# Kernel optimization log

Measured on AMD Instinct MI355X. Metric: run time of the kernel, lower is better.

The kernel has to match this reference:

```python
import jax, jax.numpy as jnp
import numpy as np
from jax import lax

B, S, H, D, NH, L, NC = 64, 512, 64, 128, 8, 4, 5
DT = 0.01

def _xavier(key, shape, gain=0.1):
    a = gain * np.sqrt(6.0 / (shape[0] + shape[1]))
    return jax.random.uniform(key, shape, jnp.float32, -a, a)

def setup_inputs():
    key = jax.random.key(0)
    ks = jax.random.split(key, 20)
    # strictly increasing positive times with spacing exactly dt -> one Euler step per interval
    times = (jnp.arange(S, dtype=jnp.float32) + 1.0) * DT
    feats = jax.random.uniform(ks[0], (B, S, 2), jnp.float32, 0.5, 5.0)
    time_series = jnp.concatenate([jnp.broadcast_to(times[None, :, None], (B, S, 1)), feats], axis=2)
    mask = jnp.ones((B, S), dtype=bool)
    noise = jax.random.normal(ks[1], (S - 1, B, H), jnp.float32)  # standard normal; scaled by sqrt(dt) inside
    n = lambda k, sh: 0.02 * jax.random.normal(k, sh, jnp.float32)
    return dict(
        time_series=time_series, mask=mask, noise=noise,
        dW1=_xavier(ks[2], (H + 1, 2 * H)), db1=jnp.zeros(2 * H, jnp.float32),
        dW2=_xavier(ks[3], (2 * H, H)), db2=jnp.zeros(H, jnp.float32),
        dW3=_xavier(ks[4], (H, H)), db3=jnp.zeros(H, jnp.float32),
        gW1=_xavier(ks[5], (H + 1, 2 * H)), gb1=jnp.zeros(2 * H, jnp.float32),
        gW2=_xavier(ks[6], (2 * H, H)), gb2=jnp.zeros(H, jnp.float32),
        min_diffusion=jnp.float32(0.05), max_drift=jnp.float32(1.0),
        in_W=n(ks[7], (H, D)), in_b=jnp.zeros(D, jnp.float32),
        Wq=n(ks[8], (L, D, D)), bq=jnp.zeros((L, D), jnp.float32),
        Wk=n(ks[9], (L, D, D)), bk=jnp.zeros((L, D), jnp.float32),
        Wv=n(ks[10], (L, D, D)), bv=jnp.zeros((L, D), jnp.float32),
        Wo=n(ks[11], (L, D, D)), bo=jnp.zeros((L, D), jnp.float32),
        ln1_s=jnp.ones((L, D), jnp.float32), ln1_b=jnp.zeros((L, D), jnp.float32),
        fW1=n(ks[12], (L, D, 4 * D)), fb1=jnp.zeros((L, 4 * D), jnp.float32),
        fW2=n(ks[13], (L, 4 * D, D)), fb2=jnp.zeros((L, D), jnp.float32),
        ln2_s=jnp.ones((L, D), jnp.float32), ln2_b=jnp.zeros((L, D), jnp.float32),
        cW1=n(ks[14], (D, D // 2)), cb1=jnp.zeros(D // 2, jnp.float32),
        cW2=n(ks[15], (D // 2, NC)), cb2=jnp.zeros(NC, jnp.float32),
    )

def _ln(x, s, b):
    m = x.mean(-1, keepdims=True)
    v = ((x - m) ** 2).mean(-1, keepdims=True)
    return (x - m) * lax.rsqrt(v + 1e-5) * s + b

def reference(time_series, mask, noise, dW1, db1, dW2, db2, dW3, db3,
              gW1, gb1, gW2, gb2, min_diffusion, max_drift,
              in_W, in_b, Wq, bq, Wk, bk, Wv, bv, Wo, bo,
              ln1_s, ln1_b, fW1, fb1, fW2, fb2, ln2_s, ln2_b,
              cW1, cb1, cW2, cb2):
    b, s = time_series.shape[:2]
    h = dW3.shape[1]
    nin = min(3, h)  # min(input_dim, hidden_channels)
    times = time_series[:, :, 0]

    # initial SDE state
    y0 = jnp.full((b, h), 0.1, time_series.dtype)
    y0 = y0.at[:, :nin].set(jnp.clip(time_series[:, 0, :nin], 0.01, 10.0))

    # per-interval left times, step sizes, Brownian increments (batch-shared time, element 0)
    ts0 = times[0]                        # (S,)
    t_left = ts0[:-1]                     # (S-1,)
    hstep = ts0[1:] - ts0[:-1]            # (S-1,)
    dW = noise * jnp.sqrt(hstep)[:, None, None]  # (S-1, B, H)

    def euler_step(y, inp):
        t, hh, dw = inp
        t_col = jnp.broadcast_to(jnp.reshape(t, (1, 1)), (y.shape[0], 1))
        ty = jnp.concatenate([y, t_col], axis=1)              # (B, H+1)
        # drift coeff net: Linear-Tanh-Linear-Tanh-Linear, clamped
        dc = jnp.tanh(ty @ dW1 + db1)
        dc = jnp.tanh(dc @ dW2 + db2)
        dc = dc @ dW3 + db3
        dc = jnp.clip(dc, -jnp.abs(max_drift), jnp.abs(max_drift))
        f = dc * y
        # diffusion coeff net: Linear-Tanh-Linear-Softplus + |min_diffusion|
        gc = jnp.tanh(ty @ gW1 + gb1)
        gc = jax.nn.softplus(gc @ gW2 + gb2) + jnp.abs(min_diffusion)
        g = gc * jnp.clip(y, -10.0, 10.0)
        y1 = jnp.clip(y + f * hh + g * dw, 0.01, 10.0)  # Euler-Maruyama + post-solve clamp
        return y1, y1

    _, traj = lax.scan(euler_step, y0, (t_left, hstep, dW))   # (S-1, B, H)
    sde_features = jnp.concatenate([y0[None], traj], axis=0).transpose(1, 0, 2)  # (B, S, H)
    mf = mask[..., None].astype(sde_features.dtype)
    sde_features = sde_features * mf

    # ContiFormer (standard post-LN transformer encoder over SDE features)
    x = sde_features @ in_W + in_b                            # (B, S, D)
    d = x.shape[-1]
    dh = d // NH
    scale = 1.0 / np.sqrt(dh)
    neg = jnp.asarray(-1e9, x.dtype)
    for l in range(Wq.shape[0]):
        q = (x @ Wq[l] + bq[l]).reshape(b, s, NH, dh)
        k = (x @ Wk[l] + bk[l]).reshape(b, s, NH, dh)
        v = (x @ Wv[l] + bv[l]).reshape(b, s, NH, dh)
        scores = jnp.einsum('bqhd,bkhd->bhqk', q, k) * scale
        scores = jnp.where(mask[:, None, None, :], scores, neg)
        attn = jax.nn.softmax(scores, axis=-1)
        o = jnp.einsum('bhqk,bkhd->bqhd', attn, v).reshape(b, s, d) @ Wo[l] + bo[l]
        x = _ln(x + o, ln1_s[l], ln1_b[l])
        ff = jax.nn.relu(x @ fW1[l] + fb1[l]) @ fW2[l] + fb2[l]
        x = _ln(x + ff, ln2_s[l], ln2_b[l])

    pooled = (x * mf).sum(1) / jnp.maximum(mf.sum(1), 1.0)    # masked mean pool (B, D)
    logits = jax.nn.relu(pooled @ cW1 + cb1) @ cW2 + cb2      # (B, NC)
    return (logits, sde_features)
```

## Files before the change

### kernel.cpp

```cpp
#include <hip/hip_runtime.h>
#include <hip/hip_bf16.h>
#include <math.h>

#define BB 64
#define SS 512
#define HH 64
#define DD 128
#define NHD 8
#define ROWS (BB*SS)

typedef unsigned short u16;
typedef __attribute__((ext_vector_type(8))) short bf16x8;
typedef __attribute__((ext_vector_type(4))) float f32x4;

__device__ __forceinline__ u16 f2b(float f) {
  union { float f; unsigned u; } x; x.f = f;
  unsigned r = x.u + 0x7fffu + ((x.u >> 16) & 1u);
  return (u16)(r >> 16);
}

__device__ __forceinline__ float b2f(u16 u) {
  return __uint_as_float(((unsigned)u) << 16);
}

__device__ __forceinline__ float fast_tanh(float x) {
  float ax = fminf(fabsf(x), 15.f);
  float e = __expf(2.f * ax);
  float r = 1.f - __fdividef(2.f, e + 1.f);
  return copysignf(r, x);
}

__device__ __forceinline__ void barrier_lds() {
  __builtin_amdgcn_s_waitcnt(0xC07F);
  __builtin_amdgcn_s_barrier();
}

__global__ __launch_bounds__(512, 2) void sde_kernel(
    const float* __restrict__ ts, const float* __restrict__ noise,
    const float* __restrict__ dW1, const float* __restrict__ db1,
    const float* __restrict__ dW2, const float* __restrict__ db2,
    const float* __restrict__ dW3, const float* __restrict__ db3,
    const float* __restrict__ gW1, const float* __restrict__ gb1,
    const float* __restrict__ gW2, const float* __restrict__ gb2,
    const float* __restrict__ pmind, const float* __restrict__ pmaxd,
    float* __restrict__ out, u16* __restrict__ outB) {
  const int b = blockIdx.x, t = threadIdx.x;
  __shared__ float y_s[64];
  __shared__ float h1g1[256];
  __shared__ float h2s[64], gcs[64];
  __shared__ float tl_s[512], hs_s[512], sq_s[512];

  const float mind = fabsf(pmind[0]);
  const float maxd = fabsf(pmaxd[0]);

  const int oA = t >> 1, hA = t & 1;
  const int cA = oA & 127;
  const float* W1 = (oA < 128) ? dW1 : gW1;
  float wA[32];
#pragma unroll
  for (int k = 0; k < 32; k++) wA[k] = W1[(hA * 32 + k) * 128 + cA];
  const float wAt = W1[64 * 128 + cA];
  const float bA = ((oA < 128) ? db1 : gb1)[cA];

  const int oB = t >> 2, qB = t & 3;
  const int cB = oB & 63;
  const float* W2 = (oB < 64) ? dW2 : gW2;
  float wB[32];
#pragma unroll
  for (int k = 0; k < 32; k++) wB[k] = W2[(qB * 32 + k) * 64 + cB];
  const float bB = ((oB < 64) ? db2 : gb2)[cB];

  const int cC = t >> 3, qC = t & 7;
  float wC[8];
#pragma unroll
  for (int k = 0; k < 8; k++) wC[k] = dW3[(qC * 8 + k) * 64 + cC];
  const float bC = db3[cC];

  tl_s[t] = ts[t * 3];
  __syncthreads();
  if (t < 511) {
    float hh = tl_s[t + 1] - tl_s[t];
    hs_s[t] = hh;
    sq_s[t] = sqrtf(hh);
  }
  if (t < 64) {
    float y = 0.1f;
    if (t < 3) y = fminf(fmaxf(ts[b * 1536 + t], 0.01f), 10.f);
    y_s[t] = y;
    out[(long)b * 32768 + t] = y;
    outB[((long)b * 512) * 64 + t] = f2b(y);
  }
  float nz = noise[b * 64 + cC];
  __syncthreads();

  for (int i = 0; i < 511; i++) {
    float nzn = 0.f;
    if (i < 510) nzn = noise[(long)(i + 1) * 4096 + b * 64 + cC];
    const float tl = tl_s[i];
    const float hh = hs_s[i];
    const float sq = sq_s[i];

    float a0 = 0.f, a1 = 0.f, a2 = 0.f, a3 = 0.f;
#pragma unroll
    for (int g = 0; g < 8; g++) {
      float4 yv = *(const float4*)&y_s[hA * 32 + g * 4];
      a0 += yv.x * wA[g * 4 + 0];
      a1 += yv.y * wA[g * 4 + 1];
      a2 += yv.z * wA[g * 4 + 2];
      a3 += yv.w * wA[g * 4 + 3];
    }
    float p1 = (a0 + a1) + (a2 + a3);
    if (hA == 0) p1 += tl * wAt + bA;
    p1 += __shfl_xor(p1, 1);
    if (hA == 0) h1g1[oA] = fast_tanh(p1);
    barrier_lds();

    const float* srcB = h1g1 + ((oB < 64) ? 0 : 128) + qB * 32;
    float c0 = 0.f, c1 = 0.f, c2 = 0.f, c3 = 0.f;
#pragma unroll
    for (int g = 0; g < 8; g++) {
      float4 xv = *(const float4*)&srcB[g * 4];
      c0 += xv.x * wB[g * 4 + 0];
      c1 += xv.y * wB[g * 4 + 1];
      c2 += xv.z * wB[g * 4 + 2];
      c3 += xv.w * wB[g * 4 + 3];
    }
    float p2 = (c0 + c1) + (c2 + c3);
    p2 += __shfl_xor(p2, 1);
    p2 += __shfl_xor(p2, 2);
    if (qB == 0) {
      p2 += bB;
      if (oB < 64) {
        h2s[cB] = fast_tanh(p2);
      } else {
        gcs[cB] = fmaxf(p2, 0.f) + __logf(1.f + __expf(-fabsf(p2))) + mind;
      }
    }
    barrier_lds();

    float d0 = 0.f, d1 = 0.f;
#pragma unroll
    for (int g = 0; g < 2; g++) {
      float4 hv = *(const float4*)&h2s[qC * 8 + g * 4];
      d0 += hv.x * wC[g * 4 + 0];
      d0 += hv.y * wC[g * 4 + 1];
      d1 += hv.z * wC[g * 4 + 2];
      d1 += hv.w * wC[g * 4 + 3];
    }
    float p3 = d0 + d1;
    p3 += __shfl_xor(p3, 1);
    p3 += __shfl_xor(p3, 2);
    p3 += __shfl_xor(p3, 4);
    if (qC == 0) {
      float dc = fminf(fmaxf(p3 + bC, -maxd), maxd);
      float yo = y_s[cC];
      float gg = gcs[cC] * fminf(fmaxf(yo, -10.f), 10.f);
      float yn = yo + dc * yo * hh + gg * nz * sq;
      yn = fminf(fmaxf(yn, 0.01f), 10.f);
      y_s[cC] = yn;
      out[(long)b * 32768 + (i + 1) * 64 + cC] = yn;
      outB[((long)b * 512 + i + 1) * 64 + cC] = f2b(yn);
    }
    nz = nzn;
    barrier_lds();
  }
}

__global__ __launch_bounds__(256) void prep_weights(
    const float* __restrict__ in_W, const float* __restrict__ Wq,
    const float* __restrict__ Wk, const float* __restrict__ Wv,
    const float* __restrict__ Wo, const float* __restrict__ fW1,
    const float* __restrict__ fW2,
    u16* __restrict__ inWt, u16* __restrict__ qkvWt, u16* __restrict__ Wot,
    u16* __restrict__ fW1t, u16* __restrict__ fW2t) {
  const int z = blockIdx.z, layer = blockIdx.y, tile = blockIdx.x;
  const float* src; u16* dst; int R, C, nl;
  switch (z) {
    case 0: src = in_W; dst = inWt; R = 64; C = 128; nl = 1; break;
    case 1: src = Wq + layer * 16384; dst = qkvWt + layer * 49152; R = 128; C = 128; nl = 4; break;
    case 2: src = Wk + layer * 16384; dst = qkvWt + layer * 49152 + 16384; R = 128; C = 128; nl = 4; break;
    case 3: src = Wv + layer * 16384; dst = qkvWt + layer * 49152 + 32768; R = 128; C = 128; nl = 4; break;
    case 4: src = Wo + layer * 16384; dst = Wot + layer * 16384; R = 128; C = 128; nl = 4; break;
    case 5: src = fW1 + layer * 65536; dst = fW1t + layer * 65536; R = 128; C = 512; nl = 4; break;
    default: src = fW2 + layer * 65536; dst = fW2t + layer * 65536; R = 512; C = 128; nl = 4; break;
  }
  const int nt = (R / 32) * (C / 32);
  if (layer >= nl || tile >= nt) return;
  const int tpr = C / 32;
  const int r0 = (tile / tpr) * 32, c0 = (tile % tpr) * 32;
  __shared__ float tl[32][33];
  const int tx = threadIdx.x & 31, ty = threadIdx.x >> 5;
#pragma unroll
  for (int p = 0; p < 4; p++)
    tl[ty + 8 * p][tx] = src[(long)(r0 + ty + 8 * p) * C + c0 + tx];
  __syncthreads();
#pragma unroll
  for (int p = 0; p < 4; p++)
    dst[(long)(c0 + ty + 8 * p) * R + r0 + tx] = f2b(tl[tx][ty + 8 * p]);
}

template <int MODE>
__global__ __launch_bounds__(256) void mfma_gemm(
    const u16* __restrict__ A, const u16* __restrict__ Bt,
    const float* __restrict__ bias, u16* __restrict__ outB, int K, int N) {
  __shared__ u16 As[128 * 40];
  __shared__ u16 Bs[64 * 40];
  const int t = threadIdx.x;
  const int nb = blockIdx.x * 64;
  const long mb = (long)blockIdx.y * 128;
  const int lane = t & 63, wave = t >> 6;
  const int wm = (wave >> 1) * 64, wn = (wave & 1) * 32;
  const int fr = lane & 15, quad = lane >> 4;

  f32x4 zero = {0.f, 0.f, 0.f, 0.f};
  f32x4 acc[4][2];
#pragma unroll
  for (int mi = 0; mi < 4; mi++)
#pragma unroll
    for (int ni = 0; ni < 2; ni++) acc[mi][ni] = zero;

  for (int k0 = 0; k0 < K; k0 += 32) {
#pragma unroll
    for (int p = 0; p < 2; p++) {
      int idx = t + p * 256, row = idx >> 2, seg = idx & 3;
      int4 v = *(const int4*)&A[(mb + row) * K + k0 + seg * 8];
      *(int4*)&As[row * 40 + seg * 8] = v;
    }
    {
      int row = t >> 2, seg = t & 3;
      int4 v = *(const int4*)&Bt[(long)(nb + row) * K + k0 + seg * 8];
      *(int4*)&Bs[row * 40 + seg * 8] = v;
    }
    __syncthreads();
    bf16x8 af[4], bfr[2];
#pragma unroll
    for (int mi = 0; mi < 4; mi++)
      af[mi] = *(const bf16x8*)&As[(wm + mi * 16 + fr) * 40 + quad * 8];
#pragma unroll
    for (int ni = 0; ni < 2; ni++)
      bfr[ni] = *(const bf16x8*)&Bs[(wn + ni * 16 + fr) * 40 + quad * 8];
#pragma unroll
    for (int mi = 0; mi < 4; mi++)
#pragma unroll
      for (int ni = 0; ni < 2; ni++)
        acc[mi][ni] = __builtin_amdgcn_mfma_f32_16x16x32_bf16(
            af[mi], bfr[ni], acc[mi][ni], 0, 0, 0);
    __syncthreads();
  }

#pragma unroll
  for (int mi = 0; mi < 4; mi++)
#pragma unroll
    for (int ni = 0; ni < 2; ni++) {
      int col = nb + wn + ni * 16 + fr;
      float bv = bias[col];
#pragma unroll
      for (int r = 0; r < 4; r++) {
        long row = mb + wm + mi * 16 + quad * 4 + r;
        float v = acc[mi][ni][r] + bv;
        if (MODE == 1) {
          outB[row * N + col] = f2b(fmaxf(v, 0.f));
        } else {
          outB[row * N + col] = f2b(v);
        }
      }
    }
}

__global__ __launch_bounds__(256) void gemm_ln(
    const u16* __restrict__ A, const u16* __restrict__ Bt,
    const float* __restrict__ bias, const u16* __restrict__ resid,
    const float* __restrict__ gamma, const float* __restrict__ beta,
    u16* __restrict__ outB, int K) {
  __shared__ u16 As[64 * 40];
  __shared__ u16 Bs[128 * 40];
  __shared__ float s1[2][64], s2[2][64];
  const int t = threadIdx.x;
  const long mb = (long)blockIdx.x * 64;
  const int lane = t & 63, wave = t >> 6;
  const int wm = (wave >> 1) * 32, wn = (wave & 1) * 64;
  const int fr = lane & 15, quad = lane >> 4;

  f32x4 zero = {0.f, 0.f, 0.f, 0.f};
  f32x4 acc[2][4];
#pragma unroll
  for (int mi = 0; mi < 2; mi++)
#pragma unroll
    for (int ni = 0; ni < 4; ni++) acc[mi][ni] = zero;

  for (int k0 = 0; k0 < K; k0 += 32) {
    {
      int row = t >> 2, seg = t & 3;
      *(int4*)&As[row * 40 + seg * 8] =
          *(const int4*)&A[(mb + row) * K + k0 + seg * 8];
    }
#pragma unroll
    for (int p = 0; p < 2; p++) {
      int idx = t + p * 256, row = idx >> 2, seg = idx & 3;
      *(int4*)&Bs[row * 40 + seg * 8] =
          *(const int4*)&Bt[(long)row * K + k0 + seg * 8];
    }
    __syncthreads();
    bf16x8 af[2], bfr[4];
#pragma unroll
    for (int mi = 0; mi < 2; mi++)
      af[mi] = *(const bf16x8*)&As[(wm + mi * 16 + fr) * 40 + quad * 8];
#pragma unroll
    for (int ni = 0; ni < 4; ni++)
      bfr[ni] = *(const bf16x8*)&Bs[(wn + ni * 16 + fr) * 40 + quad * 8];
#pragma unroll
    for (int mi = 0; mi < 2; mi++)
#pragma unroll
      for (int ni = 0; ni < 4; ni++)
        acc[mi][ni] = __builtin_amdgcn_mfma_f32_16x16x32_bf16(
            af[mi], bfr[ni], acc[mi][ni], 0, 0, 0);
    __syncthreads();
  }

  float bv[4], gv[4], be[4];
#pragma unroll
  for (int ni = 0; ni < 4; ni++) {
    int col = wn + ni * 16 + fr;
    bv[ni] = bias[col];
    gv[ni] = gamma[col];
    be[ni] = beta[col];
  }

#pragma unroll
  for (int mi = 0; mi < 2; mi++) {
#pragma unroll
    for (int r = 0; r < 4; r++) {
      int rloc = wm + mi * 16 + quad * 4 + r;
      long row = mb + rloc;
      float s = 0.f, ss = 0.f;
#pragma unroll
      for (int ni = 0; ni < 4; ni++) {
        int col = wn + ni * 16 + fr;
        float v = acc[mi][ni][r] + bv[ni] + b2f(resid[row * DD + col]);
        acc[mi][ni][r] = v;
        s += v;
        ss += v * v;
      }
      s += __shfl_xor(s, 1); ss += __shfl_xor(ss, 1);
      s += __shfl_xor(s, 2); ss += __shfl_xor(ss, 2);
      s += __shfl_xor(s, 4); ss += __shfl_xor(ss, 4);
      s += __shfl_xor(s, 8); ss += __shfl_xor(ss, 8);
      if (fr == 0) {
        s1[wn >> 6][rloc] = s;
        s2[wn >> 6][rloc] = ss;
      }
    }
  }
  __syncthreads();

#pragma unroll
  for (int mi = 0; mi < 2; mi++) {
#pragma unroll
    for (int r = 0; r < 4; r++) {
      int rloc = wm + mi * 16 + quad * 4 + r;
      long row = mb + rloc;
      float sum = s1[0][rloc] + s1[1][rloc];
      float sumsq = s2[0][rloc] + s2[1][rloc];
      float mean = sum * (1.f / 128.f);
      float var = sumsq * (1.f / 128.f) - mean * mean;
      float rstd = rsqrtf(var + 1e-5f);
#pragma unroll
      for (int ni = 0; ni < 4; ni++) {
        int col = wn + ni * 16 + fr;
        float o = (acc[mi][ni][r] - mean) * rstd * gv[ni] + be[ni];
        outB[row * DD + col] = f2b(o);
      }
    }
  }
}

__global__ __launch_bounds__(256, 2) void qkv_attn(
    const u16* __restrict__ xb, const u16* __restrict__ qkvW,
    const float* __restrict__ bq, const float* __restrict__ bk,
    const float* __restrict__ bv, u16* __restrict__ Og) {
  const int bh = blockIdx.x;
  const int b = bh >> 3, h = bh & 7;
  __shared__ u16 Ks[512 * 24];
  __shared__ u16 Vt[16 * 520];
  __shared__ u16 Qs[512 * 24];
  const int t = threadIdx.x;
  const int w = t >> 6, lane = t & 63;
  const int fr = lane & 15, quad = lane >> 4;
  const long obase = ((long)b * SS) * DD + h * 16;
  const u16* xrow = xb + (long)b * SS * DD;

  const u16* Wq_h = qkvW + (h * 16) * 128;
  const u16* Wk_h = qkvW + 16384 + (h * 16) * 128;
  const u16* Wv_h = qkvW + 32768 + (h * 16) * 128;
  bf16x8 wqf[4], wkf[4], wvf[4];
#pragma unroll
  for (int c = 0; c < 4; c++) {
    wqf[c] = *(const bf16x8*)&Wq_h[fr * 128 + c * 32 + quad * 8];
    wkf[c] = *(const bf16x8*)&Wk_h[fr * 128 + c * 32 + quad * 8];
    wvf[c] = *(const bf16x8*)&Wv_h[fr * 128 + c * 32 + quad * 8];
  }
  const float bqv = bq[h * 16 + fr];
  const float bkv = bk[h * 16 + fr];
  const float bvv = bv[h * 16 + fr];
  const f32x4 z4 = {0.f, 0.f, 0.f, 0.f};

  for (int tile = w; tile < 32; tile += 4) {
    const int t0 = tile * 16;
    bf16x8 af[4];
#pragma unroll
    for (int c = 0; c < 4; c++)
      af[c] = *(const bf16x8*)&xrow[(t0 + fr) * 128 + c * 32 + quad * 8];
    f32x4 qa = z4, ka = z4, va = z4;
#pragma unroll
    for (int c = 0; c < 4; c++) {
      qa = __builtin_amdgcn_mfma_f32_16x16x32_bf16(af[c], wqf[c], qa, 0, 0, 0);
      ka = __builtin_amdgcn_mfma_f32_16x16x32_bf16(af[c], wkf[c], ka, 0, 0, 0);
      va = __builtin_amdgcn_mfma_f32_16x16x32_bf16(af[c], wvf[c], va, 0, 0, 0);
    }
#pragma unroll
    for (int r = 0; r < 4; r++) {
      int row = t0 + quad * 4 + r;
      Qs[row * 24 + fr] = f2b(qa[r] + bqv);
      Ks[row * 24 + fr] = f2b(ka[r] + bkv);
      Vt[fr * 520 + row] = f2b(va[r] + bvv);
    }
  }
  __syncthreads();

  const float scale = 0.25f;
  const int addrA = (((quad & 1) * 32) + fr) * 4;
  const int addrB = addrA + 64;
  const bool loTile = (quad < 2);

  for (int qt = w; qt < 32; qt += 4) {
    const int q0 = qt * 16;
    bf16x8 qf = {0, 0, 0, 0, 0, 0, 0, 0};
    if (quad < 2)
      qf = *(const bf16x8*)&Qs[(q0 + fr) * 24 + quad * 8];
    f32x4 oacc = {0.f, 0.f, 0.f, 0.f};
    float mrun = -1e30f, lrun = 0.f;

    for (int kt = 0; kt < 16; kt++) {
      const int k0 = kt * 32;
      bf16x8 kf0 = {0, 0, 0, 0, 0, 0, 0, 0};
      bf16x8 kf1 = {0, 0, 0, 0, 0, 0, 0, 0};
      if (quad < 2) {
        kf0 = *(const bf16x8*)&Ks[(k0 + fr) * 24 + quad * 8];
        kf1 = *(const bf16x8*)&Ks[(k0 + 16 + fr) * 24 + quad * 8];
      }
      f32x4 slo = __builtin_amdgcn_mfma_f32_16x16x32_bf16(kf0, qf, z4, 0, 0, 0);
      f32x4 shi = __builtin_amdgcn_mfma_f32_16x16x32_bf16(kf1, qf, z4, 0, 0, 0);
      float s[8];
#pragma unroll
      for (int r = 0; r < 4; r++) {
        s[r] = slo[r] * scale;
        s[4 + r] = shi[r] * scale;
      }
      float mx = s[0];
#pragma unroll
      for (int r = 1; r < 8; r++) mx = fmaxf(mx, s[r]);
      mx = fmaxf(mx, __shfl_xor(mx, 16));
      mx = fmaxf(mx, __shfl_xor(mx, 32));
      float nm = fmaxf(mrun, mx);
      float alpha = __expf(mrun - nm);
      mrun = nm;
      float p[8], rs = 0.f;
#pragma unroll
      for (int r = 0; r < 8; r++) {
        p[r] = __expf(s[r] - nm);
        rs += p[r];
      }
      rs += __shfl_xor(rs, 16);
      rs += __shfl_xor(rs, 32);
      lrun = lrun * alpha + rs;
#pragma unroll
      for (int r = 0; r < 4; r++) oacc[r] *= alpha;

      int pk0 = ((int)f2b(p[1]) << 16) | f2b(p[0]);
      int pk1 = ((int)f2b(p[3]) << 16) | f2b(p[2]);
      int pk2 = ((int)f2b(p[5]) << 16) | f2b(p[4]);
      int pk3 = ((int)f2b(p[7]) << 16) | f2b(p[6]);
      int B0a = __builtin_amdgcn_ds_bpermute(addrA, pk0);
      int B0b = __builtin_amdgcn_ds_bpermute(addrA, pk2);
      int B1a = __builtin_amdgcn_ds_bpermute(addrA, pk1);
      int B1b = __builtin_amdgcn_ds_bpermute(addrA, pk3);
      int B2a = __builtin_amdgcn_ds_bpermute(addrB, pk0);
      int B2b = __builtin_amdgcn_ds_bpermute(addrB, pk2);
      int B3a = __builtin_amdgcn_ds_bpermute(addrB, pk1);
      int B3b = __builtin_amdgcn_ds_bpermute(addrB, pk3);
      union { int i[4]; bf16x8 v; } pu;
      pu.i[0] = loTile ? B0a : B0b;
      pu.i[1] = loTile ? B1a : B1b;
      pu.i[2] = loTile ? B2a : B2b;
      pu.i[3] = loTile ? B3a : B3b;
      bf16x8 vf = *(const bf16x8*)&Vt[fr * 520 + k0 + quad * 8];
      oacc = __builtin_amdgcn_mfma_f32_16x16x32_bf16(vf, pu.v, oacc, 0, 0, 0);
    }

    float inv = __fdividef(1.f, lrun);
    ushort4 o;
    o.x = f2b(oacc[0] * inv);
    o.y = f2b(oacc[1] * inv);
    o.z = f2b(oacc[2] * inv);
    o.w = f2b(oacc[3] * inv);
    *(ushort4*)&Og[obase + (long)(q0 + fr) * DD + quad * 4] = o;
  }
}

__global__ __launch_bounds__(128) void pool_kernel(const u16* __restrict__ X,
                                                   float* __restrict__ P) {
  const int b = blockIdx.x, c = threadIdx.x;
  float acc = 0.f;
  for (int s = 0; s < SS; s++) acc += b2f(X[((long)b * SS + s) * DD + c]);
  P[b * DD + c] = acc * (1.f / 512.f);
}

__global__ __launch_bounds__(64) void cls_kernel(
    const float* __restrict__ P, const float* __restrict__ W1,
    const float* __restrict__ b1, const float* __restrict__ W2,
    const float* __restrict__ b2, float* __restrict__ L) {
  const int b = blockIdx.x, t = threadIdx.x;
  __shared__ float sp[128];
  __shared__ float sh[64];
  sp[t] = P[b * DD + t];
  sp[t + 64] = P[b * DD + 64 + t];
  __syncthreads();
  float acc = b1[t];
  for (int k = 0; k < 128; k++) acc += sp[k] * W1[k * 64 + t];
  sh[t] = fmaxf(acc, 0.f);
  __syncthreads();
  if (t < 5) {
    float acc2 = b2[t];
    for (int k = 0; k < 64; k++) acc2 += sh[k] * W2[k * 5 + t];
    L[b * 5 + t] = acc2;
  }
}

extern "C" void kernel_launch(void* const* d_in, const int* in_sizes, int n_in,
                              void* d_out, int out_size, void* d_ws, size_t ws_size,
                              hipStream_t stream) {
  const float* ts    = (const float*)d_in[0];
  const float* noise = (const float*)d_in[2];
  const float* dW1   = (const float*)d_in[3];
  const float* db1   = (const float*)d_in[4];
  const float* dW2   = (const float*)d_in[5];
  const float* db2   = (const float*)d_in[6];
  const float* dW3   = (const float*)d_in[7];
  const float* db3   = (const float*)d_in[8];
  const float* gW1   = (const float*)d_in[9];
  const float* gb1   = (const float*)d_in[10];
  const float* gW2   = (const float*)d_in[11];
  const float* gb2   = (const float*)d_in[12];
  const float* mind  = (const float*)d_in[13];
  const float* maxd  = (const float*)d_in[14];
  const float* in_W  = (const float*)d_in[15];
  const float* in_b  = (const float*)d_in[16];
  const float* Wq    = (const float*)d_in[17];
  const float* bq    = (const float*)d_in[18];
  const float* Wk    = (const float*)d_in[19];
  const float* bk    = (const float*)d_in[20];
  const float* Wv    = (const float*)d_in[21];
  const float* bv    = (const float*)d_in[22];
  const float* Wo    = (const float*)d_in[23];
  const float* bo    = (const float*)d_in[24];
  const float* ln1s  = (const float*)d_in[25];
  const float* ln1b  = (const float*)d_in[26];
  const float* fW1   = (const float*)d_in[27];
  const float* fb1   = (const float*)d_in[28];
  const float* fW2   = (const float*)d_in[29];
  const float* fb2   = (const float*)d_in[30];
  const float* ln2s  = (const float*)d_in[31];
  const float* ln2b  = (const float*)d_in[32];
  const float* cW1   = (const float*)d_in[33];
  const float* cb1   = (const float*)d_in[34];
  const float* cW2   = (const float*)d_in[35];
  const float* cb2   = (const float*)d_in[36];

  float* logits = (float*)d_out;
  float* sde    = logits + BB * 5;

  char* W = (char*)d_ws;
  u16*  bxb    = (u16*)(W);
  u16*  bh     = (u16*)(W + (8u << 20));
  u16*  bob    = (u16*)(W + (40u << 20));
  u16*  bsb    = (u16*)(W + (48u << 20));
  u16*  wts    = (u16*)(W + (52u << 20));
  float* bp    = (float*)(W + (54u << 20));

  u16* inWt  = wts;
  u16* qkvWt = inWt + 8192;
  u16* Wot   = qkvWt + 196608;
  u16* fW1t  = Wot + 65536;
  u16* fW2t  = fW1t + 262144;

  prep_weights<<<dim3(64, 4, 7), 256, 0, stream>>>(in_W, Wq, Wk, Wv, Wo, fW1, fW2,
                                                   inWt, qkvWt, Wot, fW1t, fW2t);

  sde_kernel<<<64, 512, 0, stream>>>(ts, noise, dW1, db1, dW2, db2, dW3, db3,
                                     gW1, gb1, gW2, gb2, mind, maxd, sde, bsb);

  mfma_gemm<3><<<dim3(2, 256), 256, 0, stream>>>(bsb, inWt, in_b, bxb, 64, 128);

  for (int l = 0; l < 4; l++) {
    qkv_attn<<<BB * NHD, 256, 0, stream>>>(bxb, qkvWt + l * 49152,
                                           bq + l * DD, bk + l * DD, bv + l * DD,
                                           bob);
    gemm_ln<<<512, 256, 0, stream>>>(bob, Wot + l * 16384, bo + l * DD, bxb,
                                     ln1s + l * DD, ln1b + l * DD, bxb, 128);
    mfma_gemm<1><<<dim3(8, 256), 256, 0, stream>>>(bxb, fW1t + l * 65536,
                                                   fb1 + l * 512, bh, 128, 512);
    gemm_ln<<<512, 256, 0, stream>>>(bh, fW2t + l * 65536, fb2 + l * DD, bxb,
                                     ln2s + l * DD, ln2b + l * DD, bxb, 512);
  }

  pool_kernel<<<BB, 128, 0, stream>>>(bxb, bp);
  cls_kernel<<<BB, 64, 0, stream>>>(bp, cW1, cb1, cW2, cb2, logits);
}
```

Measured before the change: 1.262 ms.

## Restructure SDE kernel into two waves with redundant drift compute and one barrier

Rewrites the sequential SDE kernel to use 128 threads (two wavefronts) instead of 512. Each wave owns one branch, drift or diffusion, holding full weight columns in registers, and both waves redundantly compute the third drift layer. This removes shuffles and cuts the per-step block barriers from three to one, relying on wave-local LDS waits and double-buffered shared arrays instead. Noise is also prefetched four steps ahead. The cost is very high register pressure (about 320 floats of weights per thread) and less parallelism per step, which risks spills or longer serial dot products.

New measurement: 2.054 ms. +62.7%, slower.

```diff
diff --git a/kernel.cpp b/kernel.cpp
--- a/kernel.cpp
+++ b/kernel.cpp
@@ -35,7 +35,11 @@
   __builtin_amdgcn_s_barrier();
 }
 
-__global__ __launch_bounds__(512, 2) void sde_kernel(
+__device__ __forceinline__ void wait_lds() {
+  __builtin_amdgcn_s_waitcnt(0xC07F);
+}
+
+__global__ __launch_bounds__(128, 1) void sde_kernel(
     const float* __restrict__ ts, const float* __restrict__ noise,
     const float* __restrict__ dW1, const float* __restrict__ db1,
     const float* __restrict__ dW2, const float* __restrict__ db2,
@@ -45,124 +49,121 @@
     const float* __restrict__ pmind, const float* __restrict__ pmaxd,
     float* __restrict__ out, u16* __restrict__ outB) {
   const int b = blockIdx.x, t = threadIdx.x;
-  __shared__ float y_s[64];
-  __shared__ float h1g1[256];
-  __shared__ float h2s[64], gcs[64];
+  const int w = t >> 6, lane = t & 63;
+
+  __shared__ float y_s[2][64];
+  __shared__ float h1s[2][128];
+  __shared__ float h2s[2][64];
+  __shared__ float gcs[2][64];
   __shared__ float tl_s[512], hs_s[512], sq_s[512];
 
   const float mind = fabsf(pmind[0]);
   const float maxd = fabsf(pmaxd[0]);
 
-  const int oA = t >> 1, hA = t & 1;
-  const int cA = oA & 127;
-  const float* W1 = (oA < 128) ? dW1 : gW1;
-  float wA[32];
-#pragma unroll
-  for (int k = 0; k < 32; k++) wA[k] = W1[(hA * 32 + k) * 128 + cA];
-  const float wAt = W1[64 * 128 + cA];
-  const float bA = ((oA < 128) ? db1 : gb1)[cA];
-
-  const int oB = t >> 2, qB = t & 3;
-  const int cB = oB & 63;
-  const float* W2 = (oB < 64) ? dW2 : gW2;
-  float wB[32];
-#pragma unroll
-  for (int k = 0; k < 32; k++) wB[k] = W2[(qB * 32 + k) * 64 + cB];
-  const float bB = ((oB < 64) ? db2 : gb2)[cB];
-
-  const int cC = t >> 3, qC = t & 7;
-  float wC[8];
-#pragma unroll
-  for (int k = 0; k < 8; k++) wC[k] = dW3[(qC * 8 + k) * 64 + cC];
-  const float bC = db3[cC];
-
-  tl_s[t] = ts[t * 3];
+  const float* W1  = w ? gW1 : dW1;
+  const float* W2  = w ? gW2 : dW2;
+  const float* b1p = w ? gb1 : db1;
+  const float* b2p = w ? gb2 : db2;
+
+  float wa0[64], wa1[64], wb[128], wc[64];
+#pragma unroll
+  for (int k = 0; k < 64; k++) wa0[k] = W1[k * 128 + lane];
+#pragma unroll
+  for (int k = 0; k < 64; k++) wa1[k] = W1[k * 128 + 64 + lane];
+  const float wt0 = W1[64 * 128 + lane];
+  const float wt1 = W1[64 * 128 + 64 + lane];
+  const float bA0 = b1p[lane], bA1 = b1p[64 + lane];
+#pragma unroll
+  for (int k = 0; k < 128; k++) wb[k] = W2[k * 64 + lane];
+  const float bB = b2p[lane];
+#pragma unroll
+  for (int k = 0; k < 64; k++) wc[k] = dW3[k * 64 + lane];
+  const float bC = db3[lane];
+
+  for (int j = t; j < 512; j += 128) tl_s[j] = ts[j * 3];
   __syncthreads();
-  if (t < 511) {
-    float hh = tl_s[t + 1] - tl_s[t];
-    hs_s[t] = hh;
-    sq_s[t] = sqrtf(hh);
-  }
-  if (t < 64) {
-    float y = 0.1f;
-    if (t < 3) y = fminf(fmaxf(ts[b * 1536 + t], 0.01f), 10.f);
-    y_s[t] = y;
-    out[(long)b * 32768 + t] = y;
-    outB[((long)b * 512) * 64 + t] = f2b(y);
-  }
-  float nz = noise[b * 64 + cC];
+  for (int j = t; j < 511; j += 128) {
+    float hh = tl_s[j + 1] - tl_s[j];
+    hs_s[j] = hh;
+    sq_s[j] = sqrtf(hh);
+  }
+
+  float y0v = 0.1f;
+  if (lane < 3) y0v = fminf(fmaxf(ts[b * 1536 + lane], 0.01f), 10.f);
+  y_s[w][lane] = y0v;
+  float ymine = y0v;
+  if (w == 0) out[(long)b * 32768 + lane] = y0v;
+  else        outB[((long)b * 512) * 64 + lane] = f2b(y0v);
+
+  const long nofs = (long)b * 64 + lane;
+  float nz0 = noise[nofs];
+  float nz1 = noise[4096 + nofs];
+  float nz2 = noise[2 * 4096 + nofs];
+  float nz3 = noise[3 * 4096 + nofs];
   __syncthreads();
 
+  float* my_y = y_s[w];
+  float* h1p  = h1s[w];
+
   for (int i = 0; i < 511; i++) {
-    float nzn = 0.f;
-    if (i < 510) nzn = noise[(long)(i + 1) * 4096 + b * 64 + cC];
+    const int buf = i & 1;
     const float tl = tl_s[i];
     const float hh = hs_s[i];
     const float sq = sq_s[i];
 
-    float a0 = 0.f, a1 = 0.f, a2 = 0.f, a3 = 0.f;
-#pragma unroll
-    for (int g = 0; g < 8; g++) {
-      float4 yv = *(const float4*)&y_s[hA * 32 + g * 4];
-      a0 += yv.x * wA[g * 4 + 0];
-      a1 += yv.y * wA[g * 4 + 1];
-      a2 += yv.z * wA[g * 4 + 2];
-      a3 += yv.w * wA[g * 4 + 3];
-    }
-    float p1 = (a0 + a1) + (a2 + a3);
-    if (hA == 0) p1 += tl * wAt + bA;
-    p1 += __shfl_xor(p1, 1);
-    if (hA == 0) h1g1[oA] = fast_tanh(p1);
+    const float nz = nz0;
+    nz0 = nz1; nz1 = nz2; nz2 = nz3;
+    if (i + 4 < 511) nz3 = noise[(long)(i + 4) * 4096 + nofs];
+
+    float a00 = 0.f, a01 = 0.f, a10 = 0.f, a11 = 0.f;
+#pragma unroll
+    for (int g = 0; g < 16; g++) {
+      float4 yv = *(const float4*)&my_y[g * 4];
+      a00 += yv.x * wa0[g * 4 + 0]; a01 += yv.y * wa0[g * 4 + 1];
+      a00 += yv.z * wa0[g * 4 + 2]; a01 += yv.w * wa0[g * 4 + 3];
+      a10 += yv.x * wa1[g * 4 + 0]; a11 += yv.y * wa1[g * 4 + 1];
+      a10 += yv.z * wa1[g * 4 + 2]; a11 += yv.w * wa1[g * 4 + 3];
+    }
+    float p0 = (a00 + a01) + tl * wt0 + bA0;
+    float p1 = (a10 + a11) + tl * wt1 + bA1;
+    h1p[lane]      = fast_tanh(p0);
+    h1p[64 + lane] = fast_tanh(p1);
+    wait_lds();
+
+    float c0 = 0.f, c1 = 0.f, c2 = 0.f, c3 = 0.f;
+#pragma unroll
+    for (int g = 0; g < 32; g++) {
+      float4 hv = *(const float4*)&h1p[g * 4];
+      c0 += hv.x * wb[g * 4 + 0]; c1 += hv.y * wb[g * 4 + 1];
+      c2 += hv.z * wb[g * 4 + 2]; c3 += hv.w * wb[g * 4 + 3];
+    }
+    float p2 = (c0 + c1) + (c2 + c3) + bB;
+    if (w == 0) {
+      h2s[buf][lane] = fast_tanh(p2);
+    } else {
+      gcs[buf][lane] =
+          fmaxf(p2, 0.f) + __logf(1.f + __expf(-fabsf(p2))) + mind;
+    }
     barrier_lds();
 
-    const float* srcB = h1g1 + ((oB < 64) ? 0 : 128) + qB * 32;
-    float c0 = 0.f, c1 = 0.f, c2 = 0.f, c3 = 0.f;
-#pragma unroll
-    for (int g = 0; g < 8; g++) {
-      float4 xv = *(const float4*)&srcB[g * 4];
-      c0 += xv.x * wB[g * 4 + 0];
-      c1 += xv.y * wB[g * 4 + 1];
-      c2 += xv.z * wB[g * 4 + 2];
-      c3 += xv.w * wB[g * 4 + 3];
-    }
-    float p2 = (c0 + c1) + (c2 + c3);
-    p2 += __shfl_xor(p2, 1);
-    p2 += __shfl_xor(p2, 2);
-    if (qB == 0) {
-      p2 += bB;
-      if (oB < 64) {
-        h2s[cB] = fast_tanh(p2);
-      } else {
-        gcs[cB] = fmaxf(p2, 0.f) + __logf(1.f + __expf(-fabsf(p2))) + mind;
-      }
-    }
-    barrier_lds();
-
-    float d0 = 0.f, d1 = 0.f;
-#pragma unroll
-    for (int g = 0; g < 2; g++) {
-      float4 hv = *(const float4*)&h2s[qC * 8 + g * 4];
-      d0 += hv.x * wC[g * 4 + 0];
-      d0 += hv.y * wC[g * 4 + 1];
-      d1 += hv.z * wC[g * 4 + 2];
-      d1 += hv.w * wC[g * 4 + 3];
-    }
-    float p3 = d0 + d1;
-    p3 += __shfl_xor(p3, 1);
-    p3 += __shfl_xor(p3, 2);
-    p3 += __shfl_xor(p3, 4);
-    if (qC == 0) {
-      float dc = fminf(fmaxf(p3 + bC, -maxd), maxd);
-      float yo = y_s[cC];
-      float gg = gcs[cC] * fminf(fmaxf(yo, -10.f), 10.f);
-      float yn = yo + dc * yo * hh + gg * nz * sq;
-      yn = fminf(fmaxf(yn, 0.01f), 10.f);
-      y_s[cC] = yn;
-      out[(long)b * 32768 + (i + 1) * 64 + cC] = yn;
-      outB[((long)b * 512 + i + 1) * 64 + cC] = f2b(yn);
-    }
-    nz = nzn;
-    barrier_lds();
+    float d0 = 0.f, d1 = 0.f, d2 = 0.f, d3 = 0.f;
+    const float* h2p = h2s[buf];
+#pragma unroll
+    for (int g = 0; g < 16; g++) {
+      float4 hv = *(const float4*)&h2p[g * 4];
+      d0 += hv.x * wc[g * 4 + 0]; d1 += hv.y * wc[g * 4 + 1];
+      d2 += hv.z * wc[g * 4 + 2]; d3 += hv.w * wc[g * 4 + 3];
+    }
+    float dc = fminf(fmaxf((d0 + d1) + (d2 + d3) + bC, -maxd), maxd);
+    float gc = gcs[buf][lane];
+    float yo = ymine;
+    float yn = yo + dc * yo * hh + gc * fminf(fmaxf(yo, -10.f), 10.f) * nz * sq;
+    yn = fminf(fmaxf(yn, 0.01f), 10.f);
+    my_y[lane] = yn;
+    ymine = yn;
+    wait_lds();
+    if (w == 0) out[(long)b * 32768 + (i + 1) * 64 + lane] = yn;
+    else        outB[((long)b * 512 + i + 1) * 64 + lane] = f2b(yn);
   }
 }
 
@@ -596,7 +597,7 @@
   prep_weights<<<dim3(64, 4, 7), 256, 0, stream>>>(in_W, Wq, Wk, Wv, Wo, fW1, fW2,
                                                    inWt, qkvWt, Wot, fW1t, fW2t);
 
-  sde_kernel<<<64, 512, 0, stream>>>(ts, noise, dW1, db1, dW2, db2, dW3, db3,
+  sde_kernel<<<64, 128, 0, stream>>>(ts, noise, dW1, db1, dW2, db2, dW3, db3,
                                      gW1, gb1, gW2, gb2, mind, maxd, sde, bsb);
 
   mfma_gemm<3><<<dim3(2, 256), 256, 0, stream>>>(bsb, inWt, in_b, bxb, 64, 128);
```

## Halve SDE block to 256 threads with wider per-thread dot products

Applied to the files above, without the earlier changes.

The sequential SDE kernel now runs 256 threads per block instead of 512, and each thread computes longer dot products held in more registers (64-wide for layers 1 and 2, 16-wide for layer 3). This removes one shuffle reduction stage per layer and the split partial sums in the first layer. The owning thread also keeps its current state value in a register rather than rereading shared memory. The aim is to shorten the latency of each of the 511 serial steps through fewer waves and fewer cross-lane ops, at the cost of more FMAs per thread on the critical path.

Result: slower. 1.332 ms (+5.5%).

```diff
diff --git a/kernel.cpp b/kernel.cpp
--- a/kernel.cpp
+++ b/kernel.cpp
@@ -35,7 +35,7 @@
   __builtin_amdgcn_s_barrier();
 }
 
-__global__ __launch_bounds__(512, 2) void sde_kernel(
+__global__ __launch_bounds__(256) void sde_kernel(
     const float* __restrict__ ts, const float* __restrict__ noise,
     const float* __restrict__ dW1, const float* __restrict__ db1,
     const float* __restrict__ dW2, const float* __restrict__ db2,
@@ -46,43 +46,45 @@
     float* __restrict__ out, u16* __restrict__ outB) {
   const int b = blockIdx.x, t = threadIdx.x;
   __shared__ float y_s[64];
-  __shared__ float h1g1[256];
+  __shared__ float h1s[256];
   __shared__ float h2s[64], gcs[64];
   __shared__ float tl_s[512], hs_s[512], sq_s[512];
 
   const float mind = fabsf(pmind[0]);
   const float maxd = fabsf(pmaxd[0]);
 
-  const int oA = t >> 1, hA = t & 1;
-  const int cA = oA & 127;
-  const float* W1 = (oA < 128) ? dW1 : gW1;
-  float wA[32];
-#pragma unroll
-  for (int k = 0; k < 32; k++) wA[k] = W1[(hA * 32 + k) * 128 + cA];
+  const int cA = t & 127;
+  const float* W1 = (t < 128) ? dW1 : gW1;
+  float wA[64];
+#pragma unroll
+  for (int k = 0; k < 64; k++) wA[k] = W1[k * 128 + cA];
   const float wAt = W1[64 * 128 + cA];
-  const float bA = ((oA < 128) ? db1 : gb1)[cA];
-
-  const int oB = t >> 2, qB = t & 3;
+  const float bA = ((t < 128) ? db1 : gb1)[cA];
+
+  const int oB = t >> 1, hB = t & 1;
   const int cB = oB & 63;
   const float* W2 = (oB < 64) ? dW2 : gW2;
-  float wB[32];
-#pragma unroll
-  for (int k = 0; k < 32; k++) wB[k] = W2[(qB * 32 + k) * 64 + cB];
+  float wB[64];
+#pragma unroll
+  for (int k = 0; k < 64; k++) wB[k] = W2[(hB * 64 + k) * 64 + cB];
   const float bB = ((oB < 64) ? db2 : gb2)[cB];
 
-  const int cC = t >> 3, qC = t & 7;
-  float wC[8];
-#pragma unroll
-  for (int k = 0; k < 8; k++) wC[k] = dW3[(qC * 8 + k) * 64 + cC];
+  const int cC = t >> 2, qC = t & 3;
+  float wC[16];
+#pragma unroll
+  for (int k = 0; k < 16; k++) wC[k] = dW3[(qC * 16 + k) * 64 + cC];
   const float bC = db3[cC];
 
-  tl_s[t] = ts[t * 3];
+  for (int j = t; j < 512; j += 256) tl_s[j] = ts[j * 3];
   __syncthreads();
-  if (t < 511) {
-    float hh = tl_s[t + 1] - tl_s[t];
-    hs_s[t] = hh;
-    sq_s[t] = sqrtf(hh);
-  }
+  for (int j = t; j < 511; j += 256) {
+    float hh = tl_s[j + 1] - tl_s[j];
+    hs_s[j] = hh;
+    sq_s[j] = sqrtf(hh);
+  }
+
+  float ymine = 0.1f;
+  if (cC < 3) ymine = fminf(fmaxf(ts[b * 1536 + cC], 0.01f), 10.f);
   if (t < 64) {
     float y = 0.1f;
     if (t < 3) y = fminf(fmaxf(ts[b * 1536 + t], 0.01f), 10.f);
@@ -90,7 +92,7 @@
     out[(long)b * 32768 + t] = y;
     outB[((long)b * 512) * 64 + t] = f2b(y);
   }
-  float nz = noise[b * 64 + cC];
+  float nz = noise[(long)b * 64 + cC];
   __syncthreads();
 
   for (int i = 0; i < 511; i++) {
@@ -102,23 +104,21 @@
 
     float a0 = 0.f, a1 = 0.f, a2 = 0.f, a3 = 0.f;
 #pragma unroll
-    for (int g = 0; g < 8; g++) {
-      float4 yv = *(const float4*)&y_s[hA * 32 + g * 4];
+    for (int g = 0; g < 16; g++) {
+      float4 yv = *(const float4*)&y_s[g * 4];
       a0 += yv.x * wA[g * 4 + 0];
       a1 += yv.y * wA[g * 4 + 1];
       a2 += yv.z * wA[g * 4 + 2];
       a3 += yv.w * wA[g * 4 + 3];
     }
-    float p1 = (a0 + a1) + (a2 + a3);
-    if (hA == 0) p1 += tl * wAt + bA;
-    p1 += __shfl_xor(p1, 1);
-    if (hA == 0) h1g1[oA] = fast_tanh(p1);
+    float p1 = (a0 + a1) + (a2 + a3) + tl * wAt + bA;
+    h1s[t] = fast_tanh(p1);
     barrier_lds();
 
-    const float* srcB = h1g1 + ((oB < 64) ? 0 : 128) + qB * 32;
+    const float* srcB = h1s + ((oB < 64) ? 0 : 128) + hB * 64;
     float c0 = 0.f, c1 = 0.f, c2 = 0.f, c3 = 0.f;
 #pragma unroll
-    for (int g = 0; g < 8; g++) {
+    for (int g = 0; g < 16; g++) {
       float4 xv = *(const float4*)&srcB[g * 4];
       c0 += xv.x * wB[g * 4 + 0];
       c1 += xv.y * wB[g * 4 + 1];
@@ -127,8 +127,7 @@
     }
     float p2 = (c0 + c1) + (c2 + c3);
     p2 += __shfl_xor(p2, 1);
-    p2 += __shfl_xor(p2, 2);
-    if (qB == 0) {
+    if (hB == 0) {
       p2 += bB;
       if (oB < 64) {
         h2s[cB] = fast_tanh(p2);
@@ -138,26 +137,25 @@
     }
     barrier_lds();
 
-    float d0 = 0.f, d1 = 0.f;
-#pragma unroll
-    for (int g = 0; g < 2; g++) {
-      float4 hv = *(const float4*)&h2s[qC * 8 + g * 4];
+    float d0 = 0.f, d1 = 0.f, d2 = 0.f, d3 = 0.f;
+#pragma unroll
+    for (int g = 0; g < 4; g++) {
+      float4 hv = *(const float4*)&h2s[qC * 16 + g * 4];
       d0 += hv.x * wC[g * 4 + 0];
-      d0 += hv.y * wC[g * 4 + 1];
-      d1 += hv.z * wC[g * 4 + 2];
-      d1 += hv.w * wC[g * 4 + 3];
-    }
-    float p3 = d0 + d1;
+      d1 += hv.y * wC[g * 4 + 1];
+      d2 += hv.z * wC[g * 4 + 2];
+      d3 += hv.w * wC[g * 4 + 3];
+    }
+    float p3 = (d0 + d1) + (d2 + d3);
     p3 += __shfl_xor(p3, 1);
     p3 += __shfl_xor(p3, 2);
-    p3 += __shfl_xor(p3, 4);
     if (qC == 0) {
       float dc = fminf(fmaxf(p3 + bC, -maxd), maxd);
-      float yo = y_s[cC];
-      float gg = gcs[cC] * fminf(fmaxf(yo, -10.f), 10.f);
-      float yn = yo + dc * yo * hh + gg * nz * sq;
+      float gg = gcs[cC] * fminf(fmaxf(ymine, -10.f), 10.f);
+      float yn = ymine + dc * ymine * hh + gg * nz * sq;
       yn = fminf(fmaxf(yn, 0.01f), 10.f);
       y_s[cC] = yn;
+      ymine = yn;
       out[(long)b * 32768 + (i + 1) * 64 + cC] = yn;
       outB[((long)b * 512 + i + 1) * 64 + cC] = f2b(yn);
     }
@@ -596,7 +594,7 @@
   prep_weights<<<dim3(64, 4, 7), 256, 0, stream>>>(in_W, Wq, Wk, Wv, Wo, fW1, fW2,
                                                    inWt, qkvWt, Wot, fW1t, fW2t);
 
-  sde_kernel<<<64, 512, 0, stream>>>(ts, noise, dW1, db1, dW2, db2, dW3, db3,
+  sde_kernel<<<64, 256, 0, stream>>>(ts, noise, dW1, db1, dW2, db2, dW3, db3,
                                      gW1, gb1, gW2, gb2, mind, maxd, sde, bsb);
 
   mfma_gemm<3><<<dim3(2, 256), 256, 0, stream>>>(bsb, inWt, in_b, bxb, 64, 128);
```
